# Optimization experiments

Hardware: AMD Instinct MI355X
Metric: run time of the kernel (lower is better)

The kernel has to match this reference:

```python
import jax, jax.numpy as jnp
import numpy as np

# init_kwargs constants
MIN_T = 0.01
MAX_T = 0.5
TGT_MIN = 0.005
TGT_MAX = 0.03
W_MIN = 15.0
W_MAX = 5.0
W_CONT = 5.0
W_SIZE = 7.0
LESION_T = 0.3


def setup_inputs() -> dict:
    key = jax.random.key(0)
    pred = jax.random.uniform(key, (16, 1, 128, 128, 128), dtype=jnp.float32)
    return {"pred": pred}


def reference(pred):
    # pred: [B, 1, D, H, W]
    s = pred[:, 0]  # [B, D, H, W]
    B = s.shape[0]
    axes = (1, 2, 3)

    # -- min/max activation penalties (per-sample threshold means) --
    act = jnp.mean((s > MIN_T).astype(s.dtype), axis=axes)          # [B]
    loss = jax.nn.relu(TGT_MIN - act) * W_MIN
    high = jnp.mean((s > MAX_T).astype(s.dtype), axis=axes)
    loss = loss + jax.nn.relu(high - TGT_MAX) * W_MAX

    # -- continuity penalty: mean abs finite differences along D,H,W --
    d_grad = jnp.mean(jnp.abs(s[:, 1:] - s[:, :-1]), axis=axes)
    h_grad = jnp.mean(jnp.abs(s[:, :, 1:] - s[:, :, :-1]), axis=axes)
    w_grad = jnp.mean(jnp.abs(s[:, :, :, 1:] - s[:, :, :, :-1]), axis=axes)
    avg_grad = (d_grad + h_grad + w_grad) / 3.0
    has_lesion = jnp.any(s > LESION_T, axis=axes)
    loss = loss + jnp.where(has_lesion, jnp.minimum(avg_grad, 1.0), 0.0) * W_CONT

    # -- size-variance penalty over masked active values (unbiased std, torch.std) --
    mask = (s > MIN_T).astype(s.dtype)
    cnt = jnp.sum(mask, axis=axes)                                   # [B]
    cnt_safe = jnp.maximum(cnt, 1.0)
    m = jnp.sum(s * mask, axis=axes) / cnt_safe                      # masked mean [B]
    sq = jnp.sum(mask * (s - m[:, None, None, None]) ** 2, axis=axes)
    gate = (act > 0.001) & (cnt > 1.0)
    var = jnp.where(gate, sq / jnp.maximum(cnt - 1.0, 1.0), 1.0)     # guard sqrt/grad when gated off
    std = jnp.sqrt(var)
    rel_std = std / (m + 1e-6)
    pen = jnp.exp(-5.0 * rel_std)
    loss = loss + jnp.where(gate, pen, 0.0) * W_SIZE

    return jnp.sum(loss) / B
```

## Files before the change

### kernel.cpp

```cpp
#include <hip/hip_runtime.h>
#include <math.h>

#define MIN_T   0.01f
#define MAX_T   0.5f
#define LESION_T 0.3f

constexpr int VOX             = 128 * 128 * 128;
constexpr int F4_PER_BATCH    = VOX / 4;
constexpr int THREADS         = 256;
constexpr int BLOCKS_PER_BATCH = 256;
constexpr int F4_PER_BLOCK    = F4_PER_BATCH / BLOCKS_PER_BATCH;
constexpr int ITERS           = F4_PER_BLOCK / THREADS;
constexpr int NB              = 16;
constexpr int NACC            = 8;

__global__ __launch_bounds__(THREADS)
void partial_kernel(const float* __restrict__ pred, double* __restrict__ acc)
{
    const int b   = blockIdx.y;
    const int blk = blockIdx.x;
    const float* __restrict__ s = pred + (size_t)b * VOX;
    const float4* __restrict__ s4 = reinterpret_cast<const float4*>(s);

    float cnt_min = 0.f, cnt_max = 0.f, sum_d = 0.f, sum_h = 0.f,
          sum_w = 0.f, sm = 0.f, sm2 = 0.f, les = 0.f;

    #pragma unroll
    for (int k = 0; k < ITERS; ++k) {
        const int f4 = blk * F4_PER_BLOCK + k * THREADS + (int)threadIdx.x;
        const int i  = f4 * 4;
        const int w0 = i & 127;
        const int h  = (i >> 7) & 127;
        const int d  = i >> 14;

        const float4 v = s4[f4];

        {
            const float xs[4] = { v.x, v.y, v.z, v.w };
            #pragma unroll
            for (int j = 0; j < 4; ++j) {
                const float x  = xs[j];
                const float mk = (x > MIN_T) ? 1.0f : 0.0f;
                cnt_min += mk;
                cnt_max += (x > MAX_T)    ? 1.0f : 0.0f;
                les     += (x > LESION_T) ? 1.0f : 0.0f;
                sm      += x * mk;
                sm2     += x * x * mk;
            }
        }

        sum_w += fabsf(v.y - v.x) + fabsf(v.z - v.y) + fabsf(v.w - v.z);
        if (w0 < 124) {
            const float nx = s[i + 4];
            sum_w += fabsf(nx - v.w);
        }
        if (h < 127) {
            const float4 vh = s4[f4 + 32];
            sum_h += fabsf(vh.x - v.x) + fabsf(vh.y - v.y) +
                     fabsf(vh.z - v.z) + fabsf(vh.w - v.w);
        }
        if (d < 127) {
            const float4 vd = s4[f4 + 4096];
            sum_d += fabsf(vd.x - v.x) + fabsf(vd.y - v.y) +
                     fabsf(vd.z - v.z) + fabsf(vd.w - v.w);
        }
    }

    float vals[NACC] = { cnt_min, cnt_max, sum_d, sum_h, sum_w, sm, sm2, les };
    #pragma unroll
    for (int vi = 0; vi < NACC; ++vi) {
        float x = vals[vi];
        #pragma unroll
        for (int off = 32; off > 0; off >>= 1)
            x += __shfl_down(x, off, 64);
        vals[vi] = x;
    }

    __shared__ float smem[4][NACC];
    const int wave = threadIdx.x >> 6;
    const int lane = threadIdx.x & 63;
    if (lane == 0) {
        #pragma unroll
        for (int vi = 0; vi < NACC; ++vi) smem[wave][vi] = vals[vi];
    }
    __syncthreads();
    if (threadIdx.x < NACC) {
        const float t = smem[0][threadIdx.x] + smem[1][threadIdx.x] +
                        smem[2][threadIdx.x] + smem[3][threadIdx.x];
        atomicAdd(&acc[(size_t)b * NACC + threadIdx.x], (double)t);
    }
}

__global__ __launch_bounds__(64)
void finalize_kernel(const double* __restrict__ acc, float* __restrict__ out)
{
    float l = 0.0f;
    if (threadIdx.x < NB) {
        const double* a = acc + (size_t)threadIdx.x * NACC;
        const double cnt    = a[0];
        const double cntmax = a[1];
        const double sd     = a[2];
        const double sh     = a[3];
        const double sw     = a[4];
        const double sm     = a[5];
        const double sm2    = a[6];
        const double les    = a[7];

        const double inv_vox = 1.0 / (double)VOX;
        const double act  = cnt    * inv_vox;
        const double high = cntmax * inv_vox;

        double loss = fmax(0.005 - act, 0.0) * 15.0
                    + fmax(high - 0.03, 0.0) * 5.0;

        const double grad_den = 127.0 * 128.0 * 128.0;
        const double avg_grad = (sd + sh + sw) / (3.0 * grad_den);
        if (les > 0.5)
            loss += fmin(avg_grad, 1.0) * 5.0;

        const double cnt_safe = fmax(cnt, 1.0);
        const double m  = sm / cnt_safe;
        double sq = sm2 - 2.0 * m * sm + m * m * cnt;
        if (sq < 0.0) sq = 0.0;

        const bool gate = (act > 0.001) && (cnt > 1.0);
        if (gate) {
            const double var     = sq / fmax(cnt - 1.0, 1.0);
            const double rel_std = sqrt(var) / (m + 1e-6);
            loss += exp(-5.0 * rel_std) * 7.0;
        }
        l = (float)loss;
    }
    #pragma unroll
    for (int off = 32; off > 0; off >>= 1)
        l += __shfl_down(l, off, 64);
    if (threadIdx.x == 0)
        out[0] = l / (float)NB;
}

extern "C" void kernel_launch(void* const* d_in, const int* in_sizes, int n_in,
                              void* d_out, int out_size, void* d_ws, size_t ws_size,
                              hipStream_t stream)
{
    const float* pred = (const float*)d_in[0];
    float* out        = (float*)d_out;
    double* acc       = (double*)d_ws;

    hipMemsetAsync(d_ws, 0, (size_t)NB * NACC * sizeof(double), stream);

    dim3 grid(BLOCKS_PER_BATCH, NB);
    partial_kernel<<<grid, THREADS, 0, stream>>>(pred, acc);
    finalize_kernel<<<1, 64, 0, stream>>>(acc, out);
}
```

Before: 209.3 us.

## Stream along depth in registers and use lane shuffles for W neighbors

Each block now owns a column of the H-W plane and walks 32 depth slices, keeping the current slice in registers so the D-direction difference reuses the previously loaded value instead of issuing a second global load. The W-boundary neighbor comes from a cross-lane shuffle instead of a scalar global load. This cuts redundant global and cache traffic at the cost of fewer blocks (1024 instead of 4096) and a serial dependent loop per thread, which may lower memory-level parallelism. The H neighbor is still loaded separately.

```diff
diff --git a/kernel.cpp b/kernel.cpp
--- a/kernel.cpp
+++ b/kernel.cpp
@@ -1,70 +1,76 @@
 #include <hip/hip_runtime.h>
 #include <math.h>
 
-#define MIN_T   0.01f
-#define MAX_T   0.5f
+#define MIN_T    0.01f
+#define MAX_T    0.5f
 #define LESION_T 0.3f
 
-constexpr int VOX             = 128 * 128 * 128;
-constexpr int F4_PER_BATCH    = VOX / 4;
-constexpr int THREADS         = 256;
-constexpr int BLOCKS_PER_BATCH = 256;
-constexpr int F4_PER_BLOCK    = F4_PER_BATCH / BLOCKS_PER_BATCH;
-constexpr int ITERS           = F4_PER_BLOCK / THREADS;
-constexpr int NB              = 16;
-constexpr int NACC            = 8;
+constexpr int NB       = 16;
+constexpr int DIM      = 128;
+constexpr int PLANE_F4 = DIM * DIM / 4;
+constexpr int VOX      = DIM * DIM * DIM;
+constexpr int THREADS  = 256;
+constexpr int HWBLKS   = PLANE_F4 / THREADS;
+constexpr int DSEGS    = 4;
+constexpr int DPS      = DIM / DSEGS;
+constexpr int NACC     = 8;
 
 __global__ __launch_bounds__(THREADS)
 void partial_kernel(const float* __restrict__ pred, double* __restrict__ acc)
 {
-    const int b   = blockIdx.y;
-    const int blk = blockIdx.x;
-    const float* __restrict__ s = pred + (size_t)b * VOX;
-    const float4* __restrict__ s4 = reinterpret_cast<const float4*>(s);
+    const int seg   = blockIdx.x;
+    const int hwblk = blockIdx.y;
+    const int b     = blockIdx.z;
+    const int tid   = (int)threadIdx.x;
+
+    const float4* __restrict__ s4 =
+        reinterpret_cast<const float4*>(pred + (size_t)b * VOX);
+
+    const int  h    = hwblk * 8 + (tid >> 5);
+    const bool do_h = (h < DIM - 1);
+    const bool do_w = ((tid & 31) != 31);
+
+    const int d0    = seg * DPS;
+    const int d_end = (seg == DSEGS - 1) ? (DIM - 1) : (d0 + DPS);
 
     float cnt_min = 0.f, cnt_max = 0.f, sum_d = 0.f, sum_h = 0.f,
           sum_w = 0.f, sm = 0.f, sm2 = 0.f, les = 0.f;
 
-    #pragma unroll
-    for (int k = 0; k < ITERS; ++k) {
-        const int f4 = blk * F4_PER_BLOCK + k * THREADS + (int)threadIdx.x;
-        const int i  = f4 * 4;
-        const int w0 = i & 127;
-        const int h  = (i >> 7) & 127;
-        const int d  = i >> 14;
+    auto process = [&](const float4& v, const float4& vh) {
+        const float xs[4] = { v.x, v.y, v.z, v.w };
+        #pragma unroll
+        for (int j = 0; j < 4; ++j) {
+            const float x  = xs[j];
+            const float mk = (x > MIN_T) ? 1.0f : 0.0f;
+            cnt_min += mk;
+            cnt_max += (x > MAX_T)    ? 1.0f : 0.0f;
+            les     += (x > LESION_T) ? 1.0f : 0.0f;
+            sm      += x * mk;
+            sm2     += x * x * mk;
+        }
+        sum_w += fabsf(v.y - v.x) + fabsf(v.z - v.y) + fabsf(v.w - v.z);
+        const float nx = __shfl_down(v.x, 1, 64);
+        if (do_w) sum_w += fabsf(nx - v.w);
+        if (do_h) sum_h += fabsf(vh.x - v.x) + fabsf(vh.y - v.y)
+                         + fabsf(vh.z - v.z) + fabsf(vh.w - v.w);
+    };
 
-        const float4 v = s4[f4];
+    const float4 zero4 = { 0.f, 0.f, 0.f, 0.f };
+    size_t base = (size_t)d0 * PLANE_F4 + hwblk * THREADS + tid;
+    float4 v  = s4[base];
+    float4 vh = do_h ? s4[base + 32] : zero4;
 
-        {
-            const float xs[4] = { v.x, v.y, v.z, v.w };
-            #pragma unroll
-            for (int j = 0; j < 4; ++j) {
-                const float x  = xs[j];
-                const float mk = (x > MIN_T) ? 1.0f : 0.0f;
-                cnt_min += mk;
-                cnt_max += (x > MAX_T)    ? 1.0f : 0.0f;
-                les     += (x > LESION_T) ? 1.0f : 0.0f;
-                sm      += x * mk;
-                sm2     += x * x * mk;
-            }
-        }
-
-        sum_w += fabsf(v.y - v.x) + fabsf(v.z - v.y) + fabsf(v.w - v.z);
-        if (w0 < 124) {
-            const float nx = s[i + 4];
-            sum_w += fabsf(nx - v.w);
-        }
-        if (h < 127) {
-            const float4 vh = s4[f4 + 32];
-            sum_h += fabsf(vh.x - v.x) + fabsf(vh.y - v.y) +
-                     fabsf(vh.z - v.z) + fabsf(vh.w - v.w);
-        }
-        if (d < 127) {
-            const float4 vd = s4[f4 + 4096];
-            sum_d += fabsf(vd.x - v.x) + fabsf(vd.y - v.y) +
-                     fabsf(vd.z - v.z) + fabsf(vd.w - v.w);
-        }
+    for (int d = d0 + 1; d <= d_end; ++d) {
+        base += PLANE_F4;
+        const float4 nv  = s4[base];
+        const float4 nvh = do_h ? s4[base + 32] : zero4;
+        process(v, vh);
+        sum_d += fabsf(nv.x - v.x) + fabsf(nv.y - v.y)
+               + fabsf(nv.z - v.z) + fabsf(nv.w - v.w);
+        v = nv; vh = nvh;
     }
+    if (seg == DSEGS - 1)
+        process(v, vh);
 
     float vals[NACC] = { cnt_min, cnt_max, sum_d, sum_h, sum_w, sm, sm2, les };
     #pragma unroll
@@ -77,17 +83,17 @@
     }
 
     __shared__ float smem[4][NACC];
-    const int wave = threadIdx.x >> 6;
-    const int lane = threadIdx.x & 63;
+    const int wave = tid >> 6;
+    const int lane = tid & 63;
     if (lane == 0) {
         #pragma unroll
         for (int vi = 0; vi < NACC; ++vi) smem[wave][vi] = vals[vi];
     }
     __syncthreads();
-    if (threadIdx.x < NACC) {
-        const float t = smem[0][threadIdx.x] + smem[1][threadIdx.x] +
-                        smem[2][threadIdx.x] + smem[3][threadIdx.x];
-        atomicAdd(&acc[(size_t)b * NACC + threadIdx.x], (double)t);
+    if (tid < NACC) {
+        const float t = smem[0][tid] + smem[1][tid] +
+                        smem[2][tid] + smem[3][tid];
+        atomicAdd(&acc[(size_t)b * NACC + tid], (double)t);
     }
 }
 
@@ -148,7 +154,7 @@
 
     hipMemsetAsync(d_ws, 0, (size_t)NB * NACC * sizeof(double), stream);
 
-    dim3 grid(BLOCKS_PER_BATCH, NB);
+    dim3 grid(DSEGS, HWBLKS, NB);
     partial_kernel<<<grid, THREADS, 0, stream>>>(pred, acc);
     finalize_kernel<<<1, 64, 0, stream>>>(acc, out);
 }
```

Result: faster. 192.9 us (-7.8%).
